# Kernel tuning notes

Measured on AMD Instinct MI355X. Metric: run time of the kernel, lower is better.

Reference implementation:

```python
import jax, jax.numpy as jnp
import numpy as np

D = 64       # embedding_dim
N = 10000    # nodes
E = 160000   # edges (avg degree 16)
R = 16       # removals
C = 512      # connected edges scored per removal


def setup_inputs() -> dict:
    key = jax.random.key(0)
    ks = jax.random.split(key, 18)
    coords = jax.random.normal(ks[0], (N, 2), jnp.float32)
    edge_src = jax.random.randint(ks[1], (E,), 0, N, jnp.int32)
    edge_dst = jax.random.randint(ks[2], (E,), 0, N, jnp.int32)
    removal_idx = jax.random.randint(ks[3], (R,), 0, N, jnp.int32)
    conn_eidx = jax.random.randint(ks[4], (R, C), 0, E, jnp.int32)
    s2 = 1.0 / np.sqrt(2.0)
    sD = 1.0 / np.sqrt(D)
    s2D = 1.0 / np.sqrt(2 * D)
    return {
        "coords": coords,
        "W_emb": jax.random.normal(ks[5], (2, D), jnp.float32) * s2,
        "b_emb": jnp.zeros((D,), jnp.float32),
        "W_self0": jax.random.normal(ks[6], (D, D), jnp.float32) * sD,
        "W_neigh0": jax.random.normal(ks[7], (D, D), jnp.float32) * sD,
        "b_gnn0": jnp.zeros((D,), jnp.float32),
        "W_self1": jax.random.normal(ks[8], (D, D), jnp.float32) * sD,
        "W_neigh1": jax.random.normal(ks[9], (D, D), jnp.float32) * sD,
        "b_gnn1": jnp.zeros((D,), jnp.float32),
        "W_edge": jax.random.normal(ks[10], (2 * D, D), jnp.float32) * s2D,
        "b_edge": jnp.zeros((D,), jnp.float32),
        "W_score": jax.random.normal(ks[11], (2 * D, 1), jnp.float32) * s2D,
        "b_score": jnp.zeros((1,), jnp.float32),
        "edge_src": edge_src,
        "edge_dst": edge_dst,
        "removal_idx": removal_idx,
        "conn_eidx": conn_eidx,
    }


def reference(coords, W_emb, b_emb, W_self0, W_neigh0, b_gnn0,
              W_self1, W_neigh1, b_gnn1, W_edge, b_edge, W_score, b_score,
              edge_src, edge_dst, removal_idx, conn_eidx):
    Nn = coords.shape[0]
    h0 = coords @ W_emb + b_emb  # [N, D] init node embedding

    def gnn_layer(h, emask, Ws, Wn, b):
        # masked mean aggregation of neighbor messages, then linear + relu
        msg = h[edge_src] * emask[:, None]                       # [E, D]
        agg = jax.ops.segment_sum(msg, edge_dst, num_segments=Nn)
        deg = jax.ops.segment_sum(emask, edge_dst, num_segments=Nn)
        agg = agg / jnp.maximum(deg, 1.0)[:, None]
        return jax.nn.relu(h @ Ws + agg @ Wn + b)

    def per_removal(r, conn):
        # tempDestroy: mask out removed node's participation in message passing
        nmask = jnp.ones((Nn,), coords.dtype).at[r].set(0.0)
        emask = nmask[edge_src] * nmask[edge_dst]                # [E]
        h = h0
        h = gnn_layer(h, emask, W_self0, W_neigh0, b_gnn0) + h   # residual
        h = gnn_layer(h, emask, W_self1, W_neigh1, b_gnn1) + h
        s, d = edge_src[conn], edge_dst[conn]                    # connected edges
        ef = jax.nn.relu(jnp.concatenate([h[s], h[d]], -1) @ W_edge + b_edge)  # [C, D]
        r_embed = coords[r] @ W_emb + b_emb                      # [D]
        score_in = jnp.concatenate(
            [jnp.broadcast_to(r_embed, (conn.shape[0], r_embed.shape[0])), ef], -1)
        score = score_in @ W_score + b_score                     # [C, 1]
        return jax.nn.softmax(score, axis=0)[:, 0]               # softmax over edges

    return jax.vmap(per_removal)(removal_idx, conn_eidx)         # [R, C]
```

## Files before the change

### kernel.cpp

```cpp
#include <hip/hip_runtime.h>

#define Df 64
#define NN 10000
#define EE 160000
#define RR 16
#define CC 512
#define CAP1 128
#define CAP2 2048
#define NGEMM 157
#define NAGG 2500
#define NEDG 625
#define NSLF 40
#define ND1B 512
#define ND2B 8192

__device__ float g_h0[NN * Df];
__device__ float g_h1b[NN * Df];
__device__ float g_h2b[NN * Df];
__device__ float g_agg[NN * Df];
__device__ float g_zrow[Df];
__device__ __align__(16) float g_W20[128 * Df];
__device__ __align__(16) float g_W21[128 * Df];
__device__ int g_cntI[NN], g_rowI[NN + 1], g_posI[NN], g_csrI[EE];
__device__ int g_m1mask[NN], g_m2mask[NN];
__device__ int g_mark1[RR][NN], g_mark2[RR][NN];
__device__ int g_n1[RR], g_n2[RR];
__device__ int g_list1[RR][CAP1], g_list2[RR][CAP2];
__device__ float g_d1[RR][CAP1][Df];
__device__ float g_d2[RR][CAP2][Df];
__device__ float g_score[RR * CC];

__global__ void k_init(const float* __restrict__ coords, const float* __restrict__ We,
                       const float* __restrict__ be, const float* __restrict__ Ws0,
                       const float* __restrict__ Wn0, const float* __restrict__ Ws1,
                       const float* __restrict__ Wn1) {
    int i = blockIdx.x * 256 + threadIdx.x;
    if (i < NN * Df) {
        int n = i >> 6, d = i & 63;
        g_h0[i] = coords[2 * n] * We[d] + coords[2 * n + 1] * We[Df + d] + be[d];
    }
    if (i < NN) { g_cntI[i] = 0; g_m1mask[i] = 0; g_m2mask[i] = 0; }
    if (i < Df) g_zrow[i] = 0.f;
    if (i < 8192) {
        int k = i >> 6, d = i & 63;
        g_W20[i] = (k < 64) ? Ws0[k * 64 + d] : Wn0[(k - 64) * 64 + d];
    } else if (i < 16384) {
        int i2 = i - 8192;
        int k = i2 >> 6, d = i2 & 63;
        g_W21[i2] = (k < 64) ? Ws1[k * 64 + d] : Wn1[(k - 64) * 64 + d];
    }
}

__global__ void k_hist(const int* __restrict__ dst) {
    int e = blockIdx.x * 256 + threadIdx.x;
    if (e < EE) atomicAdd(&g_cntI[dst[e]], 1);
}

__global__ __launch_bounds__(1024) void k_scan() {
    int t = threadIdx.x;
    int lane = t & 63, wv = t >> 6;
    const int PER = 10;
    int base = t * PER;
    int vals[PER]; int loc = 0;
#pragma unroll
    for (int k = 0; k < PER; k++) { int v = base + k; vals[k] = (v < NN) ? g_cntI[v] : 0; loc += vals[k]; }
    int sc = loc;
#pragma unroll
    for (int off = 1; off < 64; off <<= 1) { int x = __shfl_up(sc, off, 64); if (lane >= off) sc += x; }
    __shared__ int wsum[16];
    if (lane == 63) wsum[wv] = sc;
    __syncthreads();
    if (t < 16) {
        int x = wsum[t]; int s2 = x;
#pragma unroll
        for (int off = 1; off < 16; off <<= 1) { int y = __shfl_up(s2, off, 16); if (t >= off) s2 += y; }
        wsum[t] = s2 - x;
    }
    __syncthreads();
    int run = wsum[wv] + (sc - loc);
#pragma unroll
    for (int k = 0; k < PER; k++) {
        int v = base + k;
        if (v < NN) { g_rowI[v] = run; g_posI[v] = run; run += vals[k]; }
    }
    if (t == 1023) g_rowI[NN] = run;
}

__global__ void k_fill(const int* __restrict__ src, const int* __restrict__ dst) {
    int e = blockIdx.x * 256 + threadIdx.x;
    if (e < EE) {
        int p = atomicAdd(&g_posI[dst[e]], 1);
        g_csrI[p] = src[e];
    }
}

__device__ __forceinline__ void compact256(const int* __restrict__ maskArr, int bit,
                                           int* mark, int* list, int* nout, int cap) {
    int t = threadIdx.x;
    int lane = t & 63, wv = t >> 6;
    const int PER = 40;
    int base = t * PER;
    int loc = 0;
    for (int k = 0; k < PER; k++) { int v = base + k; if (v < NN) loc += (maskArr[v] >> bit) & 1; }
    int sc = loc;
#pragma unroll
    for (int off = 1; off < 64; off <<= 1) { int x = __shfl_up(sc, off, 64); if (lane >= off) sc += x; }
    __shared__ int wsum[4];
    if (lane == 63) wsum[wv] = sc;
    __syncthreads();
    if (t == 0) { int a = 0; for (int w2 = 0; w2 < 4; w2++) { int x = wsum[w2]; wsum[w2] = a; a += x; } }
    __syncthreads();
    int run = wsum[wv] + (sc - loc);
    for (int k = 0; k < PER; k++) {
        int v = base + k;
        if (v < NN) {
            int f = (maskArr[v] >> bit) & 1;
            if (f && run < cap) { list[run] = v; mark[v] = run + 1; }
            else mark[v] = 0;
            run += f;
        }
    }
    if (t == 255) *nout = (run < cap) ? run : cap;
}

__device__ __forceinline__ void agg_quad(const float* __restrict__ hin, int b, int tid) {
    int lane = tid & 63, w = tid >> 6;
    int n = b * 4 + w;
    int a0 = g_rowI[n], a1 = g_rowI[n + 1];
    float s0 = 0.f, s1 = 0.f, s2 = 0.f, s3 = 0.f;
    int i = a0;
    for (; i + 4 <= a1; i += 4) {
        int c0 = g_csrI[i], c1 = g_csrI[i + 1], c2 = g_csrI[i + 2], c3 = g_csrI[i + 3];
        s0 += hin[c0 * Df + lane];
        s1 += hin[c1 * Df + lane];
        s2 += hin[c2 * Df + lane];
        s3 += hin[c3 * Df + lane];
    }
    for (; i < a1; i++) s0 += hin[g_csrI[i] * Df + lane];
    float s = (s0 + s1) + (s2 + s3);
    g_agg[n * Df + lane] = s / fmaxf((float)(a1 - a0), 1.f);
}

__device__ __forceinline__ void gemm_tile(const float* __restrict__ hin,
                                          float* __restrict__ hout,
                                          const float* __restrict__ W2,
                                          const float* __restrict__ bias, int m0,
                                          int tid) {
    __shared__ float Xs[32][68];
    __shared__ float Wl[32][64];
    int tx = tid & 15, ty = tid >> 4;
    float acc[4][4];
#pragma unroll
    for (int i = 0; i < 4; i++)
#pragma unroll
        for (int j = 0; j < 4; j++) acc[i][j] = 0.f;

    for (int c = 0; c < 4; c++) {
        const float* src = (c < 2) ? hin : g_agg;
        int kb = (c & 1) * 32;
        int kbase = c * 32;
#pragma unroll
        for (int rep = 0; rep < 2; rep++) {
            int slot = tid + rep * 256;
            int m = slot >> 3, q = slot & 7;
            int n = m0 + m;
            float4 v = make_float4(0.f, 0.f, 0.f, 0.f);
            if (n < NN) v = *(const float4*)&src[n * Df + kb + q * 4];
            Xs[q * 4 + 0][m] = v.x; Xs[q * 4 + 1][m] = v.y;
            Xs[q * 4 + 2][m] = v.z; Xs[q * 4 + 3][m] = v.w;
            int k = slot >> 4, dq = slot & 15;
            *(float4*)&Wl[k][dq * 4] = *(const float4*)&W2[(kbase + k) * Df + dq * 4];
        }
        __syncthreads();
#pragma unroll
        for (int k = 0; k < 32; k++) {
            float4 x4 = *(const float4*)&Xs[k][ty * 4];
            float4 w4 = *(const float4*)&Wl[k][tx * 4];
            float xs[4] = {x4.x, x4.y, x4.z, x4.w};
            float ws[4] = {w4.x, w4.y, w4.z, w4.w};
#pragma unroll
            for (int i = 0; i < 4; i++)
#pragma unroll
                for (int j = 0; j < 4; j++) acc[i][j] += xs[i] * ws[j];
        }
        __syncthreads();
    }
    float4 b4 = *(const float4*)&bias[tx * 4];
    float bb[4] = {b4.x, b4.y, b4.z, b4.w};
#pragma unroll
    for (int i = 0; i < 4; i++) {
        int n = m0 + ty * 4 + i;
        if (n < NN) {
            float4 hv = *(const float4*)&hin[n * Df + tx * 4];
            float4 o;
            o.x = fmaxf(acc[i][0] + bb[0], 0.f) + hv.x;
            o.y = fmaxf(acc[i][1] + bb[1], 0.f) + hv.y;
            o.z = fmaxf(acc[i][2] + bb[2], 0.f) + hv.z;
            o.w = fmaxf(acc[i][3] + bb[3], 0.f) + hv.w;
            *(float4*)&hout[n * Df + tx * 4] = o;
        }
    }
}

__global__ __launch_bounds__(256) void k_s1(const int* __restrict__ removal,
                                            const int* __restrict__ esrc,
                                            const int* __restrict__ edst) {
    int b = blockIdx.x, tid = threadIdx.x;
    if (b < NAGG) { agg_quad(g_h0, b, tid); return; }
    if (b < NAGG + NEDG) {
        int e = (b - NAGG) * 256 + tid;
        if (e < EE) {
            int s = esrc[e], d = edst[e];
            int m = 0;
#pragma unroll
            for (int ri = 0; ri < RR; ri++)
                if (s == removal[ri]) m |= (1 << ri);
            if (m) atomicOr(&g_m1mask[d], m);
        }
        return;
    }
    if (tid < RR) atomicOr(&g_m1mask[removal[tid]], 1 << tid);
}

__global__ __launch_bounds__(256) void k_s2(const float* __restrict__ b0,
                                            const int* __restrict__ esrc,
                                            const int* __restrict__ edst) {
    int b = blockIdx.x, tid = threadIdx.x;
    if (b < NGEMM) { gemm_tile(g_h0, g_h1b, g_W20, b0, b * 64, tid); return; }
    if (b < NGEMM + RR) {
        int ri = b - NGEMM;
        compact256(g_m1mask, ri, g_mark1[ri], g_list1[ri], &g_n1[ri], CAP1);
        return;
    }
    if (b < NGEMM + RR + NEDG) {
        int e = (b - NGEMM - RR) * 256 + tid;
        if (e < EE) {
            int m = g_m1mask[esrc[e]];
            if (m) atomicOr(&g_m2mask[edst[e]], m);
        }
        return;
    }
    int v = (b - NGEMM - RR - NEDG) * 256 + tid;
    if (v < NN) {
        int m = g_m1mask[v];
        if (m) atomicOr(&g_m2mask[v], m);
    }
}

__global__ __launch_bounds__(256) void k_s3(const int* __restrict__ removal,
        const float* __restrict__ Ws0, const float* __restrict__ Wn0,
        const float* __restrict__ b0) {
    int b = blockIdx.x, tid = threadIdx.x;
    if (b < NAGG) { agg_quad(g_h1b, b, tid); return; }
    if (b < NAGG + ND1B) {
        __shared__ float s_h[4][Df], s_a[4][Df];
        int rel = b - NAGG;
        int ri = rel >> 5, y = rel & 31;
        int lane = tid & 63, w = tid >> 6;
        int j = y * 4 + w;
        if (j >= g_n1[ri]) return;
        int v = g_list1[ri][j];
        int r = removal[ri];
        float p0s = 0.f, p1s = 0.f, p2s = 0.f, p3s = 0.f; int cnt = 0;
        if (v != r) {
            int e0 = g_rowI[v], e1 = g_rowI[v + 1];
            int i = e0;
            for (; i + 4 <= e1; i += 4) {
                int c0 = g_csrI[i], c1 = g_csrI[i + 1], c2 = g_csrI[i + 2], c3 = g_csrI[i + 3];
                const float* p0 = (c0 == r) ? g_zrow : &g_h0[c0 * Df];
                const float* p1 = (c1 == r) ? g_zrow : &g_h0[c1 * Df];
                const float* p2 = (c2 == r) ? g_zrow : &g_h0[c2 * Df];
                const float* p3 = (c3 == r) ? g_zrow : &g_h0[c3 * Df];
                p0s += p0[lane]; p1s += p1[lane]; p2s += p2[lane]; p3s += p3[lane];
                cnt += (c0 != r) + (c1 != r) + (c2 != r) + (c3 != r);
            }
            for (; i < e1; i++) {
                int c = g_csrI[i];
                const float* p = (c == r) ? g_zrow : &g_h0[c * Df];
                p0s += p[lane]; cnt += (c != r);
            }
        }
        float aggd = (p0s + p1s) + (p2s + p3s);
        float hv = g_h0[v * Df + lane];
        s_h[w][lane] = hv;
        s_a[w][lane] = aggd / fmaxf((float)cnt, 1.f);
        float acc = b0[lane];
#pragma unroll 16
        for (int k = 0; k < Df; k++)
            acc += s_h[w][k] * Ws0[k * Df + lane] + s_a[w][k] * Wn0[k * Df + lane];
        g_d1[ri][j][lane] = fmaxf(acc, 0.f) + hv;
        return;
    }
    int ri = b - NAGG - ND1B;
    compact256(g_m2mask, ri, g_mark2[ri], g_list2[ri], &g_n2[ri], CAP2);
}

__global__ __launch_bounds__(256) void k_s4(const int* __restrict__ removal,
        const float* __restrict__ Ws1, const float* __restrict__ Wn1,
        const float* __restrict__ b1) {
    int b = blockIdx.x, tid = threadIdx.x;
    if (b < NGEMM) { gemm_tile(g_h1b, g_h2b, g_W21, b1, b * 64, tid); return; }
    __shared__ float s_h[4][Df], s_a[4][Df];
    int rel = b - NGEMM;
    int ri = rel >> 9, y = rel & 511;
    int lane = tid & 63, w = tid >> 6;
    int j = y * 4 + w;
    if (j >= g_n2[ri]) return;
    int v = g_list2[ri][j];
    int r = removal[ri];
    const int* mk1 = g_mark1[ri];
    float p0s = 0.f, p1s = 0.f, p2s = 0.f, p3s = 0.f; int cnt = 0;
    if (v != r) {
        int e0 = g_rowI[v], e1 = g_rowI[v + 1];
        int i = e0;
        for (; i + 4 <= e1; i += 4) {
            int c0 = g_csrI[i], c1 = g_csrI[i + 1], c2 = g_csrI[i + 2], c3 = g_csrI[i + 3];
            int m0 = mk1[c0], m1 = mk1[c1], m2 = mk1[c2], m3 = mk1[c3];
            const float* p0 = (c0 == r) ? g_zrow : (m0 > 0 ? &g_d1[ri][m0 - 1][0] : &g_h1b[c0 * Df]);
            const float* p1 = (c1 == r) ? g_zrow : (m1 > 0 ? &g_d1[ri][m1 - 1][0] : &g_h1b[c1 * Df]);
            const float* p2 = (c2 == r) ? g_zrow : (m2 > 0 ? &g_d1[ri][m2 - 1][0] : &g_h1b[c2 * Df]);
            const float* p3 = (c3 == r) ? g_zrow : (m3 > 0 ? &g_d1[ri][m3 - 1][0] : &g_h1b[c3 * Df]);
            p0s += p0[lane]; p1s += p1[lane]; p2s += p2[lane]; p3s += p3[lane];
            cnt += (c0 != r) + (c1 != r) + (c2 != r) + (c3 != r);
        }
        for (; i < e1; i++) {
            int c = g_csrI[i];
            int m = mk1[c];
            const float* p = (c == r) ? g_zrow : (m > 0 ? &g_d1[ri][m - 1][0] : &g_h1b[c * Df]);
            p0s += p[lane]; cnt += (c != r);
        }
    }
    float aggd = (p0s + p1s) + (p2s + p3s);
    int mv = mk1[v];
    float hv = (mv > 0) ? g_d1[ri][mv - 1][lane] : g_h1b[v * Df + lane];
    s_h[w][lane] = hv;
    s_a[w][lane] = aggd / fmaxf((float)cnt, 1.f);
    float acc = b1[lane];
#pragma unroll 16
    for (int k = 0; k < Df; k++)
        acc += s_h[w][k] * Ws1[k * Df + lane] + s_a[w][k] * Wn1[k * Df + lane];
    g_d2[ri][j][lane] = fmaxf(acc, 0.f) + hv;
}

__global__ __launch_bounds__(256) void k_score(const int* __restrict__ conn,
        const int* __restrict__ removal, const int* __restrict__ esrc,
        const int* __restrict__ edst, const float* __restrict__ We,
        const float* __restrict__ be, const float* __restrict__ Wsc,
        const float* __restrict__ bsc) {
    __shared__ const float* ptrs[128];
    __shared__ float Xs[32][68];
    __shared__ float Wl[32][64];
    __shared__ float su;
    int tid = threadIdx.x;
    int e0 = blockIdx.x * 64;
    int ri = e0 >> 9;

    if (tid < 64) {
        int e = conn[e0 + tid];
        int s = esrc[e], d = edst[e];
        int ms = g_mark2[ri][s], md = g_mark2[ri][d];
        ptrs[tid]      = (ms > 0) ? &g_d2[ri][ms - 1][0] : &g_h2b[s * Df];
        ptrs[64 + tid] = (md > 0) ? &g_d2[ri][md - 1][0] : &g_h2b[d * Df];
    } else if (tid < 128) {
        int lane = tid & 63;
        float up = g_h0[removal[ri] * Df + lane] * Wsc[lane];
#pragma unroll
        for (int off = 32; off > 0; off >>= 1) up += __shfl_xor(up, off, 64);
        if (lane == 0) su = up;
    }
    __syncthreads();

    int tx = tid & 15, ty = tid >> 4;
    float acc[4][4];
#pragma unroll
    for (int i = 0; i < 4; i++)
#pragma unroll
        for (int j = 0; j < 4; j++) acc[i][j] = 0.f;

    for (int c = 0; c < 4; c++) {
        int kb = (c & 1) * 32;
#pragma unroll
        for (int rep = 0; rep < 2; rep++) {
            int slot = tid + rep * 256;
            int m = slot >> 3, q = slot & 7;
            const float* p = ((c < 2) ? ptrs[m] : ptrs[64 + m]) + kb + q * 4;
            float4 v = *(const float4*)p;
            Xs[q * 4 + 0][m] = v.x; Xs[q * 4 + 1][m] = v.y;
            Xs[q * 4 + 2][m] = v.z; Xs[q * 4 + 3][m] = v.w;
            int k = slot >> 4, dq = slot & 15;
            *(float4*)&Wl[k][dq * 4] = *(const float4*)&We[(c * 32 + k) * Df + dq * 4];
        }
        __syncthreads();
#pragma unroll
        for (int k = 0; k < 32; k++) {
            float4 x4 = *(const float4*)&Xs[k][ty * 4];
            float4 w4 = *(const float4*)&Wl[k][tx * 4];
            float xs[4] = {x4.x, x4.y, x4.z, x4.w};
            float ws[4] = {w4.x, w4.y, w4.z, w4.w};
#pragma unroll
            for (int i = 0; i < 4; i++)
#pragma unroll
                for (int j = 0; j < 4; j++) acc[i][j] += xs[i] * ws[j];
        }
        __syncthreads();
    }

    float4 be4 = *(const float4*)&be[tx * 4];
    float4 w2  = *(const float4*)&Wsc[Df + tx * 4];
    float bb[4] = {be4.x, be4.y, be4.z, be4.w};
    float ww[4] = {w2.x, w2.y, w2.z, w2.w};
    float sb = su + bsc[0];
#pragma unroll
    for (int i = 0; i < 4; i++) {
        float part = 0.f;
#pragma unroll
        for (int j = 0; j < 4; j++) part += fmaxf(acc[i][j] + bb[j], 0.f) * ww[j];
#pragma unroll
        for (int off = 1; off < 16; off <<= 1) part += __shfl_xor(part, off, 64);
        if (tx == 0) g_score[e0 + ty * 4 + i] = part + sb;
    }
}

__global__ void k_softmax(float* __restrict__ out) {
    int r = blockIdx.x;
    int t = threadIdx.x;
    float v0 = g_score[r * CC + t];
    float v1 = g_score[r * CC + 256 + t];
    __shared__ float red[256];
    red[t] = fmaxf(v0, v1);
    __syncthreads();
    for (int off = 128; off > 0; off >>= 1) {
        if (t < off) red[t] = fmaxf(red[t], red[t + off]);
        __syncthreads();
    }
    float mx = red[0];
    __syncthreads();
    float e0 = expf(v0 - mx), e1 = expf(v1 - mx);
    red[t] = e0 + e1;
    __syncthreads();
    for (int off = 128; off > 0; off >>= 1) {
        if (t < off) red[t] += red[t + off];
        __syncthreads();
    }
    float inv = 1.f / red[0];
    out[r * CC + t] = e0 * inv;
    out[r * CC + 256 + t] = e1 * inv;
}

extern "C" void kernel_launch(void* const* d_in, const int* in_sizes, int n_in,
                              void* d_out, int out_size, void* d_ws, size_t ws_size,
                              hipStream_t stream) {
    const float* coords   = (const float*)d_in[0];
    const float* W_emb    = (const float*)d_in[1];
    const float* b_emb    = (const float*)d_in[2];
    const float* W_self0  = (const float*)d_in[3];
    const float* W_neigh0 = (const float*)d_in[4];
    const float* b_gnn0   = (const float*)d_in[5];
    const float* W_self1  = (const float*)d_in[6];
    const float* W_neigh1 = (const float*)d_in[7];
    const float* b_gnn1   = (const float*)d_in[8];
    const float* W_edge   = (const float*)d_in[9];
    const float* b_edge   = (const float*)d_in[10];
    const float* W_score  = (const float*)d_in[11];
    const float* b_score  = (const float*)d_in[12];
    const int* esrc       = (const int*)d_in[13];
    const int* edst       = (const int*)d_in[14];
    const int* removal    = (const int*)d_in[15];
    const int* conn       = (const int*)d_in[16];

    k_init<<<2500, 256, 0, stream>>>(coords, W_emb, b_emb, W_self0, W_neigh0,
                                     W_self1, W_neigh1);
    k_hist<<<NEDG, 256, 0, stream>>>(edst);
    k_scan<<<1, 1024, 0, stream>>>();
    k_fill<<<NEDG, 256, 0, stream>>>(esrc, edst);

    k_s1<<<NAGG + NEDG + 1, 256, 0, stream>>>(removal, esrc, edst);
    k_s2<<<NGEMM + RR + NEDG + NSLF, 256, 0, stream>>>(b_gnn0, esrc, edst);
    k_s3<<<NAGG + ND1B + RR, 256, 0, stream>>>(removal, W_self0, W_neigh0, b_gnn0);
    k_s4<<<NGEMM + ND2B, 256, 0, stream>>>(removal, W_self1, W_neigh1, b_gnn1);

    k_score<<<RR * CC / 64, 256, 0, stream>>>(conn, removal, esrc, edst,
                                              W_edge, b_edge, W_score, b_score);
    k_softmax<<<RR, 256, 0, stream>>>((float*)d_out);
}
```

Before: 132.8 us.

## Replace CSR build with fixed-width per-node buckets and regroup stage kernels

Drops the histogram, scan and fill passes that built the CSR adjacency. Incoming edges now go straight into fixed 128-slot buckets per destination node through one atomic counter, fused with the removal-mask flagging. The stage kernels are regrouped so the layer-0 aggregation runs earlier, the layer-1 GEMM becomes its own launch, and the gather loop is widened to 8 independent accumulators. This removes several launches and a serial scan, at the cost of a large padded bucket array and silent truncation for any node with more than 128 in-edges. The degree divisor still uses the full count, so truncated nodes would be scaled wrongly.

After: 126.7 us (median of 2 runs). 1.05x faster.

```diff
diff --git a/kernel.cpp b/kernel.cpp
--- a/kernel.cpp
+++ b/kernel.cpp
@@ -7,6 +7,7 @@
 #define CC 512
 #define CAP1 128
 #define CAP2 2048
+#define BST 128
 #define NGEMM 157
 #define NAGG 2500
 #define NEDG 625
@@ -21,7 +22,8 @@
 __device__ float g_zrow[Df];
 __device__ __align__(16) float g_W20[128 * Df];
 __device__ __align__(16) float g_W21[128 * Df];
-__device__ int g_cntI[NN], g_rowI[NN + 1], g_posI[NN], g_csrI[EE];
+__device__ int g_deg[NN];
+__device__ __align__(16) int g_bkt[NN * BST];
 __device__ int g_m1mask[NN], g_m2mask[NN];
 __device__ int g_mark1[RR][NN], g_mark2[RR][NN];
 __device__ int g_n1[RR], g_n2[RR];
@@ -30,72 +32,8 @@
 __device__ float g_d2[RR][CAP2][Df];
 __device__ float g_score[RR * CC];
 
-__global__ void k_init(const float* __restrict__ coords, const float* __restrict__ We,
-                       const float* __restrict__ be, const float* __restrict__ Ws0,
-                       const float* __restrict__ Wn0, const float* __restrict__ Ws1,
-                       const float* __restrict__ Wn1) {
-    int i = blockIdx.x * 256 + threadIdx.x;
-    if (i < NN * Df) {
-        int n = i >> 6, d = i & 63;
-        g_h0[i] = coords[2 * n] * We[d] + coords[2 * n + 1] * We[Df + d] + be[d];
-    }
-    if (i < NN) { g_cntI[i] = 0; g_m1mask[i] = 0; g_m2mask[i] = 0; }
-    if (i < Df) g_zrow[i] = 0.f;
-    if (i < 8192) {
-        int k = i >> 6, d = i & 63;
-        g_W20[i] = (k < 64) ? Ws0[k * 64 + d] : Wn0[(k - 64) * 64 + d];
-    } else if (i < 16384) {
-        int i2 = i - 8192;
-        int k = i2 >> 6, d = i2 & 63;
-        g_W21[i2] = (k < 64) ? Ws1[k * 64 + d] : Wn1[(k - 64) * 64 + d];
-    }
-}
-
-__global__ void k_hist(const int* __restrict__ dst) {
-    int e = blockIdx.x * 256 + threadIdx.x;
-    if (e < EE) atomicAdd(&g_cntI[dst[e]], 1);
-}
-
-__global__ __launch_bounds__(1024) void k_scan() {
-    int t = threadIdx.x;
-    int lane = t & 63, wv = t >> 6;
-    const int PER = 10;
-    int base = t * PER;
-    int vals[PER]; int loc = 0;
-#pragma unroll
-    for (int k = 0; k < PER; k++) { int v = base + k; vals[k] = (v < NN) ? g_cntI[v] : 0; loc += vals[k]; }
-    int sc = loc;
-#pragma unroll
-    for (int off = 1; off < 64; off <<= 1) { int x = __shfl_up(sc, off, 64); if (lane >= off) sc += x; }
-    __shared__ int wsum[16];
-    if (lane == 63) wsum[wv] = sc;
-    __syncthreads();
-    if (t < 16) {
-        int x = wsum[t]; int s2 = x;
-#pragma unroll
-        for (int off = 1; off < 16; off <<= 1) { int y = __shfl_up(s2, off, 16); if (t >= off) s2 += y; }
-        wsum[t] = s2 - x;
-    }
-    __syncthreads();
-    int run = wsum[wv] + (sc - loc);
-#pragma unroll
-    for (int k = 0; k < PER; k++) {
-        int v = base + k;
-        if (v < NN) { g_rowI[v] = run; g_posI[v] = run; run += vals[k]; }
-    }
-    if (t == 1023) g_rowI[NN] = run;
-}
-
-__global__ void k_fill(const int* __restrict__ src, const int* __restrict__ dst) {
-    int e = blockIdx.x * 256 + threadIdx.x;
-    if (e < EE) {
-        int p = atomicAdd(&g_posI[dst[e]], 1);
-        g_csrI[p] = src[e];
-    }
-}
-
-__device__ __forceinline__ void compact256(const int* __restrict__ maskArr, int bit,
-                                           int* mark, int* list, int* nout, int cap) {
+__device__ void compact256(const int* __restrict__ maskArr, int bit,
+                           int* mark, int* list, int* nout, int cap) {
     int t = threadIdx.x;
     int lane = t & 63, wv = t >> 6;
     const int PER = 40;
@@ -105,12 +43,12 @@
     int sc = loc;
 #pragma unroll
     for (int off = 1; off < 64; off <<= 1) { int x = __shfl_up(sc, off, 64); if (lane >= off) sc += x; }
-    __shared__ int wsum[4];
-    if (lane == 63) wsum[wv] = sc;
-    __syncthreads();
-    if (t == 0) { int a = 0; for (int w2 = 0; w2 < 4; w2++) { int x = wsum[w2]; wsum[w2] = a; a += x; } }
-    __syncthreads();
-    int run = wsum[wv] + (sc - loc);
+    __shared__ int wsumC[4];
+    if (lane == 63) wsumC[wv] = sc;
+    __syncthreads();
+    if (t == 0) { int a = 0; for (int w2 = 0; w2 < 4; w2++) { int x = wsumC[w2]; wsumC[w2] = a; a += x; } }
+    __syncthreads();
+    int run = wsumC[wv] + (sc - loc);
     for (int k = 0; k < PER; k++) {
         int v = base + k;
         if (v < NN) {
@@ -121,33 +59,40 @@
         }
     }
     if (t == 255) *nout = (run < cap) ? run : cap;
-}
-
-__device__ __forceinline__ void agg_quad(const float* __restrict__ hin, int b, int tid) {
+    __syncthreads();
+}
+
+__device__ void agg8(const float* __restrict__ hin, int b, int tid) {
     int lane = tid & 63, w = tid >> 6;
     int n = b * 4 + w;
-    int a0 = g_rowI[n], a1 = g_rowI[n + 1];
+    int deg = g_deg[n];
+    int dg = deg < BST ? deg : BST;
+    const int* bp = &g_bkt[n * BST];
     float s0 = 0.f, s1 = 0.f, s2 = 0.f, s3 = 0.f;
-    int i = a0;
-    for (; i + 4 <= a1; i += 4) {
-        int c0 = g_csrI[i], c1 = g_csrI[i + 1], c2 = g_csrI[i + 2], c3 = g_csrI[i + 3];
-        s0 += hin[c0 * Df + lane];
-        s1 += hin[c1 * Df + lane];
-        s2 += hin[c2 * Df + lane];
-        s3 += hin[c3 * Df + lane];
-    }
-    for (; i < a1; i++) s0 += hin[g_csrI[i] * Df + lane];
-    float s = (s0 + s1) + (s2 + s3);
-    g_agg[n * Df + lane] = s / fmaxf((float)(a1 - a0), 1.f);
-}
-
-__device__ __forceinline__ void gemm_tile(const float* __restrict__ hin,
-                                          float* __restrict__ hout,
-                                          const float* __restrict__ W2,
-                                          const float* __restrict__ bias, int m0,
-                                          int tid) {
-    __shared__ float Xs[32][68];
-    __shared__ float Wl[32][64];
+    float s4 = 0.f, s5 = 0.f, s6 = 0.f, s7 = 0.f;
+    int i = 0;
+    for (; i + 8 <= dg; i += 8) {
+        int4 a = *(const int4*)&bp[i];
+        int4 c = *(const int4*)&bp[i + 4];
+        s0 += hin[a.x * Df + lane];
+        s1 += hin[a.y * Df + lane];
+        s2 += hin[a.z * Df + lane];
+        s3 += hin[a.w * Df + lane];
+        s4 += hin[c.x * Df + lane];
+        s5 += hin[c.y * Df + lane];
+        s6 += hin[c.z * Df + lane];
+        s7 += hin[c.w * Df + lane];
+    }
+    for (; i < dg; i++) s0 += hin[bp[i] * Df + lane];
+    float s = ((s0 + s1) + (s2 + s3)) + ((s4 + s5) + (s6 + s7));
+    g_agg[n * Df + lane] = s / fmaxf((float)deg, 1.f);
+}
+
+__device__ void gemm_tile(const float* __restrict__ hin, float* __restrict__ hout,
+                          const float* __restrict__ W2, const float* __restrict__ bias,
+                          int m0, int tid, char* smem) {
+    float (*Xs)[68] = (float(*)[68])smem;
+    float (*Wl)[64] = (float(*)[64])(smem + 8704);
     int tx = tid & 15, ty = tid >> 4;
     float acc[4][4];
 #pragma unroll
@@ -202,106 +147,54 @@
     }
 }
 
-__global__ __launch_bounds__(256) void k_s1(const int* __restrict__ removal,
-                                            const int* __restrict__ esrc,
-                                            const int* __restrict__ edst) {
-    int b = blockIdx.x, tid = threadIdx.x;
-    if (b < NAGG) { agg_quad(g_h0, b, tid); return; }
-    if (b < NAGG + NEDG) {
-        int e = (b - NAGG) * 256 + tid;
-        if (e < EE) {
-            int s = esrc[e], d = edst[e];
-            int m = 0;
-#pragma unroll
-            for (int ri = 0; ri < RR; ri++)
-                if (s == removal[ri]) m |= (1 << ri);
-            if (m) atomicOr(&g_m1mask[d], m);
-        }
-        return;
-    }
-    if (tid < RR) atomicOr(&g_m1mask[removal[tid]], 1 << tid);
-}
-
-__global__ __launch_bounds__(256) void k_s2(const float* __restrict__ b0,
-                                            const int* __restrict__ esrc,
-                                            const int* __restrict__ edst) {
-    int b = blockIdx.x, tid = threadIdx.x;
-    if (b < NGEMM) { gemm_tile(g_h0, g_h1b, g_W20, b0, b * 64, tid); return; }
-    if (b < NGEMM + RR) {
-        int ri = b - NGEMM;
-        compact256(g_m1mask, ri, g_mark1[ri], g_list1[ri], &g_n1[ri], CAP1);
-        return;
-    }
-    if (b < NGEMM + RR + NEDG) {
-        int e = (b - NGEMM - RR) * 256 + tid;
-        if (e < EE) {
-            int m = g_m1mask[esrc[e]];
-            if (m) atomicOr(&g_m2mask[edst[e]], m);
-        }
-        return;
-    }
-    int v = (b - NGEMM - RR - NEDG) * 256 + tid;
-    if (v < NN) {
-        int m = g_m1mask[v];
-        if (m) atomicOr(&g_m2mask[v], m);
-    }
-}
-
-__global__ __launch_bounds__(256) void k_s3(const int* __restrict__ removal,
-        const float* __restrict__ Ws0, const float* __restrict__ Wn0,
-        const float* __restrict__ b0) {
-    int b = blockIdx.x, tid = threadIdx.x;
-    if (b < NAGG) { agg_quad(g_h1b, b, tid); return; }
-    if (b < NAGG + ND1B) {
-        __shared__ float s_h[4][Df], s_a[4][Df];
-        int rel = b - NAGG;
-        int ri = rel >> 5, y = rel & 31;
-        int lane = tid & 63, w = tid >> 6;
-        int j = y * 4 + w;
-        if (j >= g_n1[ri]) return;
-        int v = g_list1[ri][j];
-        int r = removal[ri];
-        float p0s = 0.f, p1s = 0.f, p2s = 0.f, p3s = 0.f; int cnt = 0;
-        if (v != r) {
-            int e0 = g_rowI[v], e1 = g_rowI[v + 1];
-            int i = e0;
-            for (; i + 4 <= e1; i += 4) {
-                int c0 = g_csrI[i], c1 = g_csrI[i + 1], c2 = g_csrI[i + 2], c3 = g_csrI[i + 3];
-                const float* p0 = (c0 == r) ? g_zrow : &g_h0[c0 * Df];
-                const float* p1 = (c1 == r) ? g_zrow : &g_h0[c1 * Df];
-                const float* p2 = (c2 == r) ? g_zrow : &g_h0[c2 * Df];
-                const float* p3 = (c3 == r) ? g_zrow : &g_h0[c3 * Df];
-                p0s += p0[lane]; p1s += p1[lane]; p2s += p2[lane]; p3s += p3[lane];
-                cnt += (c0 != r) + (c1 != r) + (c2 != r) + (c3 != r);
-            }
-            for (; i < e1; i++) {
-                int c = g_csrI[i];
-                const float* p = (c == r) ? g_zrow : &g_h0[c * Df];
-                p0s += p[lane]; cnt += (c != r);
-            }
-        }
-        float aggd = (p0s + p1s) + (p2s + p3s);
-        float hv = g_h0[v * Df + lane];
-        s_h[w][lane] = hv;
-        s_a[w][lane] = aggd / fmaxf((float)cnt, 1.f);
-        float acc = b0[lane];
+__device__ void delta1_blk(int rel, int tid, const int* __restrict__ removal,
+                           const float* __restrict__ Ws, const float* __restrict__ Wn,
+                           const float* __restrict__ bias, char* smem) {
+    float* s_h = (float*)smem;
+    float* s_a = s_h + 4 * Df;
+    int ri = rel >> 5, y = rel & 31;
+    int lane = tid & 63, w = tid >> 6;
+    int j = y * 4 + w;
+    if (j >= g_n1[ri]) return;
+    int v = g_list1[ri][j];
+    int r = removal[ri];
+    float p0s = 0.f, p1s = 0.f, p2s = 0.f, p3s = 0.f; int cnt = 0;
+    if (v != r) {
+        int deg = g_deg[v];
+        int dg = deg < BST ? deg : BST;
+        const int* bp = &g_bkt[v * BST];
+        int i = 0;
+        for (; i + 4 <= dg; i += 4) {
+            int c0 = bp[i], c1 = bp[i + 1], c2 = bp[i + 2], c3 = bp[i + 3];
+            const float* p0 = (c0 == r) ? g_zrow : &g_h0[c0 * Df];
+            const float* p1 = (c1 == r) ? g_zrow : &g_h0[c1 * Df];
+            const float* p2 = (c2 == r) ? g_zrow : &g_h0[c2 * Df];
+            const float* p3 = (c3 == r) ? g_zrow : &g_h0[c3 * Df];
+            p0s += p0[lane]; p1s += p1[lane]; p2s += p2[lane]; p3s += p3[lane];
+            cnt += (c0 != r) + (c1 != r) + (c2 != r) + (c3 != r);
+        }
+        for (; i < dg; i++) {
+            int c = bp[i];
+            const float* p = (c == r) ? g_zrow : &g_h0[c * Df];
+            p0s += p[lane]; cnt += (c != r);
+        }
+    }
+    float aggd = (p0s + p1s) + (p2s + p3s);
+    float hv = g_h0[v * Df + lane];
+    s_h[w * Df + lane] = hv;
+    s_a[w * Df + lane] = aggd / fmaxf((float)cnt, 1.f);
+    float acc = bias[lane];
 #pragma unroll 16
-        for (int k = 0; k < Df; k++)
-            acc += s_h[w][k] * Ws0[k * Df + lane] + s_a[w][k] * Wn0[k * Df + lane];
-        g_d1[ri][j][lane] = fmaxf(acc, 0.f) + hv;
-        return;
-    }
-    int ri = b - NAGG - ND1B;
-    compact256(g_m2mask, ri, g_mark2[ri], g_list2[ri], &g_n2[ri], CAP2);
-}
-
-__global__ __launch_bounds__(256) void k_s4(const int* __restrict__ removal,
-        const float* __restrict__ Ws1, const float* __restrict__ Wn1,
-        const float* __restrict__ b1) {
-    int b = blockIdx.x, tid = threadIdx.x;
-    if (b < NGEMM) { gemm_tile(g_h1b, g_h2b, g_W21, b1, b * 64, tid); return; }
-    __shared__ float s_h[4][Df], s_a[4][Df];
-    int rel = b - NGEMM;
+    for (int k = 0; k < Df; k++)
+        acc += s_h[w * Df + k] * Ws[k * Df + lane] + s_a[w * Df + k] * Wn[k * Df + lane];
+    g_d1[ri][j][lane] = fmaxf(acc, 0.f) + hv;
+}
+
+__device__ void delta2_blk(int rel, int tid, const int* __restrict__ removal,
+                           const float* __restrict__ Ws, const float* __restrict__ Wn,
+                           const float* __restrict__ bias, char* smem) {
+    float* s_h = (float*)smem;
+    float* s_a = s_h + 4 * Df;
     int ri = rel >> 9, y = rel & 511;
     int lane = tid & 63, w = tid >> 6;
     int j = y * 4 + w;
@@ -311,10 +204,12 @@
     const int* mk1 = g_mark1[ri];
     float p0s = 0.f, p1s = 0.f, p2s = 0.f, p3s = 0.f; int cnt = 0;
     if (v != r) {
-        int e0 = g_rowI[v], e1 = g_rowI[v + 1];
-        int i = e0;
-        for (; i + 4 <= e1; i += 4) {
-            int c0 = g_csrI[i], c1 = g_csrI[i + 1], c2 = g_csrI[i + 2], c3 = g_csrI[i + 3];
+        int deg = g_deg[v];
+        int dg = deg < BST ? deg : BST;
+        const int* bp = &g_bkt[v * BST];
+        int i = 0;
+        for (; i + 4 <= dg; i += 4) {
+            int c0 = bp[i], c1 = bp[i + 1], c2 = bp[i + 2], c3 = bp[i + 3];
             int m0 = mk1[c0], m1 = mk1[c1], m2 = mk1[c2], m3 = mk1[c3];
             const float* p0 = (c0 == r) ? g_zrow : (m0 > 0 ? &g_d1[ri][m0 - 1][0] : &g_h1b[c0 * Df]);
             const float* p1 = (c1 == r) ? g_zrow : (m1 > 0 ? &g_d1[ri][m1 - 1][0] : &g_h1b[c1 * Df]);
@@ -323,8 +218,8 @@
             p0s += p0[lane]; p1s += p1[lane]; p2s += p2[lane]; p3s += p3[lane];
             cnt += (c0 != r) + (c1 != r) + (c2 != r) + (c3 != r);
         }
-        for (; i < e1; i++) {
-            int c = g_csrI[i];
+        for (; i < dg; i++) {
+            int c = bp[i];
             int m = mk1[c];
             const float* p = (c == r) ? g_zrow : (m > 0 ? &g_d1[ri][m - 1][0] : &g_h1b[c * Df]);
             p0s += p[lane]; cnt += (c != r);
@@ -333,13 +228,101 @@
     float aggd = (p0s + p1s) + (p2s + p3s);
     int mv = mk1[v];
     float hv = (mv > 0) ? g_d1[ri][mv - 1][lane] : g_h1b[v * Df + lane];
-    s_h[w][lane] = hv;
-    s_a[w][lane] = aggd / fmaxf((float)cnt, 1.f);
-    float acc = b1[lane];
+    s_h[w * Df + lane] = hv;
+    s_a[w * Df + lane] = aggd / fmaxf((float)cnt, 1.f);
+    float acc = bias[lane];
 #pragma unroll 16
     for (int k = 0; k < Df; k++)
-        acc += s_h[w][k] * Ws1[k * Df + lane] + s_a[w][k] * Wn1[k * Df + lane];
+        acc += s_h[w * Df + k] * Ws[k * Df + lane] + s_a[w * Df + k] * Wn[k * Df + lane];
     g_d2[ri][j][lane] = fmaxf(acc, 0.f) + hv;
+}
+
+__global__ void k_init(const float* __restrict__ coords, const float* __restrict__ We,
+                       const float* __restrict__ be, const float* __restrict__ Ws0,
+                       const float* __restrict__ Wn0, const float* __restrict__ Ws1,
+                       const float* __restrict__ Wn1) {
+    int i = blockIdx.x * 256 + threadIdx.x;
+    if (i < NN * Df) {
+        int n = i >> 6, d = i & 63;
+        g_h0[i] = coords[2 * n] * We[d] + coords[2 * n + 1] * We[Df + d] + be[d];
+    }
+    if (i < NN) { g_deg[i] = 0; g_m1mask[i] = 0; g_m2mask[i] = 0; }
+    if (i < Df) g_zrow[i] = 0.f;
+    if (i < 8192) {
+        int k = i >> 6, d = i & 63;
+        g_W20[i] = (k < 64) ? Ws0[k * 64 + d] : Wn0[(k - 64) * 64 + d];
+        g_W21[i] = (k < 64) ? Ws1[k * 64 + d] : Wn1[(k - 64) * 64 + d];
+    }
+}
+
+__global__ void k_fillflag(const int* __restrict__ esrc, const int* __restrict__ edst,
+                           const int* __restrict__ removal) {
+    __shared__ int s_rem[RR];
+    int tid = threadIdx.x;
+    if (tid < RR) s_rem[tid] = removal[tid];
+    __syncthreads();
+    int e = blockIdx.x * 256 + tid;
+    if (e < EE) {
+        int s = esrc[e], d = edst[e];
+        int p = atomicAdd(&g_deg[d], 1);
+        if (p < BST) g_bkt[d * BST + p] = s;
+        int m = 0;
+#pragma unroll
+        for (int ri = 0; ri < RR; ri++)
+            if (s == s_rem[ri]) m |= (1 << ri);
+        if (m) atomicOr(&g_m1mask[d], m);
+    }
+    if (blockIdx.x == 0 && tid < RR)
+        atomicOr(&g_m1mask[removal[tid]], 1 << tid);
+}
+
+__global__ __launch_bounds__(256) void k_L3(const int* __restrict__ esrc,
+                                            const int* __restrict__ edst) {
+    int b = blockIdx.x, tid = threadIdx.x;
+    if (b < NAGG) { agg8(g_h0, b, tid); return; }
+    if (b < NAGG + NEDG) {
+        int e = (b - NAGG) * 256 + tid;
+        if (e < EE) {
+            int m = g_m1mask[esrc[e]];
+            if (m) atomicOr(&g_m2mask[edst[e]], m);
+        }
+        return;
+    }
+    if (b < NAGG + NEDG + NSLF) {
+        int v = (b - NAGG - NEDG) * 256 + tid;
+        if (v < NN) {
+            int m = g_m1mask[v];
+            if (m) atomicOr(&g_m2mask[v], m);
+        }
+        return;
+    }
+    int ri = b - NAGG - NEDG - NSLF;
+    compact256(g_m1mask, ri, g_mark1[ri], g_list1[ri], &g_n1[ri], CAP1);
+}
+
+__global__ __launch_bounds__(256) void k_L4(const int* __restrict__ removal,
+        const float* __restrict__ Ws0, const float* __restrict__ Wn0,
+        const float* __restrict__ b0) {
+    __shared__ __align__(16) char smem[16896];
+    int b = blockIdx.x, tid = threadIdx.x;
+    if (b < NGEMM) { gemm_tile(g_h0, g_h1b, g_W20, b0, b * 64, tid, smem); return; }
+    if (b < NGEMM + ND1B) { delta1_blk(b - NGEMM, tid, removal, Ws0, Wn0, b0, smem); return; }
+    int ri = b - NGEMM - ND1B;
+    compact256(g_m2mask, ri, g_mark2[ri], g_list2[ri], &g_n2[ri], CAP2);
+}
+
+__global__ __launch_bounds__(256) void k_L5(const int* __restrict__ removal,
+        const float* __restrict__ Ws1, const float* __restrict__ Wn1,
+        const float* __restrict__ b1) {
+    __shared__ __align__(16) char smem[2048];
+    int b = blockIdx.x, tid = threadIdx.x;
+    if (b < NAGG) { agg8(g_h1b, b, tid); return; }
+    delta2_blk(b - NAGG, tid, removal, Ws1, Wn1, b1, smem);
+}
+
+__global__ __launch_bounds__(256) void k_gemm1(const float* __restrict__ b1) {
+    __shared__ __align__(16) char smem[16896];
+    gemm_tile(g_h1b, g_h2b, g_W21, b1, blockIdx.x * 64, threadIdx.x, smem);
 }
 
 __global__ __launch_bounds__(256) void k_score(const int* __restrict__ conn,
@@ -470,15 +453,11 @@
 
     k_init<<<2500, 256, 0, stream>>>(coords, W_emb, b_emb, W_self0, W_neigh0,
                                      W_self1, W_neigh1);
-    k_hist<<<NEDG, 256, 0, stream>>>(edst);
-    k_scan<<<1, 1024, 0, stream>>>();
-    k_fill<<<NEDG, 256, 0, stream>>>(esrc, edst);
-
-    k_s1<<<NAGG + NEDG + 1, 256, 0, stream>>>(removal, esrc, edst);
-    k_s2<<<NGEMM + RR + NEDG + NSLF, 256, 0, stream>>>(b_gnn0, esrc, edst);
-    k_s3<<<NAGG + ND1B + RR, 256, 0, stream>>>(removal, W_self0, W_neigh0, b_gnn0);
-    k_s4<<<NGEMM + ND2B, 256, 0, stream>>>(removal, W_self1, W_neigh1, b_gnn1);
-
+    k_fillflag<<<NEDG, 256, 0, stream>>>(esrc, edst, removal);
+    k_L3<<<NAGG + NEDG + NSLF + RR, 256, 0, stream>>>(esrc, edst);
+    k_L4<<<NGEMM + ND1B + RR, 256, 0, stream>>>(removal, W_self0, W_neigh0, b_gnn0);
+    k_L5<<<NAGG + ND2B, 256, 0, stream>>>(removal, W_self1, W_neigh1, b_gnn1);
+    k_gemm1<<<NGEMM, 256, 0, stream>>>(b_gnn1);
     k_score<<<RR * CC / 64, 256, 0, stream>>>(conn, removal, esrc, edst,
                                               W_edge, b_edge, W_score, b_score);
     k_softmax<<<RR, 256, 0, stream>>>((float*)d_out);
```
